# Kernel tuning notes

Hardware: AMD Instinct MI355X
Metric: run time of the kernel (lower is better)

## Reference

```python
import jax, jax.numpy as jnp
import numpy as np

INPUT_DIM = 29
OUTPUT_DIM = 67
ES = 256
HS = 512
SRC_LEN = 64
TRG_LEN = 48
BATCH = 512


def _lstm_cell(x, h, c, Wih, Whh, bih, bhh):
    # PyTorch gate order: i, f, g, o
    g = x @ Wih.T + bih + h @ Whh.T + bhh
    i, f, gg, o = jnp.split(g, 4, axis=-1)
    c_new = jax.nn.sigmoid(f) * c + jax.nn.sigmoid(i) * jnp.tanh(gg)
    h_new = jax.nn.sigmoid(o) * jnp.tanh(c_new)
    return h_new, c_new


def setup_inputs() -> dict:
    key = jax.random.key(0)
    ks = jax.random.split(key, 32)
    s_es = 1.0 / np.sqrt(ES)
    s_hs = 1.0 / np.sqrt(HS)
    inp = {}
    inp['src'] = jax.random.randint(ks[0], (SRC_LEN, BATCH), 0, INPUT_DIM)
    inp['trg'] = jax.random.randint(ks[1], (TRG_LEN, BATCH), 0, OUTPUT_DIM)
    # encoder params
    inp['enc_emb'] = jax.random.normal(ks[2], (INPUT_DIM, ES), jnp.float32)
    inp['enc_Wih_f'] = jax.random.normal(ks[3], (4 * HS, ES), jnp.float32) * s_hs
    inp['enc_Whh_f'] = jax.random.normal(ks[4], (4 * HS, HS), jnp.float32) * s_hs
    inp['enc_bih_f'] = jax.random.normal(ks[5], (4 * HS,), jnp.float32) * s_hs
    inp['enc_bhh_f'] = jax.random.normal(ks[6], (4 * HS,), jnp.float32) * s_hs
    inp['enc_Wih_b'] = jax.random.normal(ks[7], (4 * HS, ES), jnp.float32) * s_hs
    inp['enc_Whh_b'] = jax.random.normal(ks[8], (4 * HS, HS), jnp.float32) * s_hs
    inp['enc_bih_b'] = jax.random.normal(ks[9], (4 * HS,), jnp.float32) * s_hs
    inp['enc_bhh_b'] = jax.random.normal(ks[10], (4 * HS,), jnp.float32) * s_hs
    inp['fc_h_W'] = jax.random.normal(ks[11], (HS, 2 * HS), jnp.float32) * s_hs
    inp['fc_h_b'] = jax.random.normal(ks[12], (HS,), jnp.float32) * s_hs
    inp['fc_c_W'] = jax.random.normal(ks[13], (HS, 2 * HS), jnp.float32) * s_hs
    inp['fc_c_b'] = jax.random.normal(ks[14], (HS,), jnp.float32) * s_hs
    # decoder params
    inp['dec_emb'] = jax.random.normal(ks[15], (OUTPUT_DIM, ES), jnp.float32)
    inp['dec_Wih'] = jax.random.normal(ks[16], (4 * HS, 2 * HS + ES), jnp.float32) * s_hs
    inp['dec_Whh'] = jax.random.normal(ks[17], (4 * HS, HS), jnp.float32) * s_hs
    inp['dec_bih'] = jax.random.normal(ks[18], (4 * HS,), jnp.float32) * s_hs
    inp['dec_bhh'] = jax.random.normal(ks[19], (4 * HS,), jnp.float32) * s_hs
    inp['energy_W'] = jax.random.normal(ks[20], (1, 3 * HS), jnp.float32) * s_hs
    inp['energy_b'] = jax.random.normal(ks[21], (1,), jnp.float32) * s_hs
    inp['fc_out_W'] = jax.random.normal(ks[22], (OUTPUT_DIM, HS), jnp.float32) * s_hs
    inp['fc_out_b'] = jax.random.normal(ks[23], (OUTPUT_DIM,), jnp.float32) * s_hs
    return inp


def _forward(src, trg, enc_emb, enc_Wih_f, enc_Whh_f, enc_bih_f, enc_bhh_f,
             enc_Wih_b, enc_Whh_b, enc_bih_b, enc_bhh_b,
             fc_h_W, fc_h_b, fc_c_W, fc_c_b,
             dec_emb, dec_Wih, dec_Whh, dec_bih, dec_bhh,
             energy_W, energy_b, fc_out_W, fc_out_b):
    S, B = src.shape
    T = trg.shape[0]
    emb = enc_emb[src]  # [S, B, ES]
    h0 = jnp.zeros((B, HS), emb.dtype)
    c0 = jnp.zeros((B, HS), emb.dtype)

    def fwd_step(carry, x_t):
        h, c = carry
        h, c = _lstm_cell(x_t, h, c, enc_Wih_f, enc_Whh_f, enc_bih_f, enc_bhh_f)
        return (h, c), h

    def bwd_step(carry, x_t):
        h, c = carry
        h, c = _lstm_cell(x_t, h, c, enc_Wih_b, enc_Whh_b, enc_bih_b, enc_bhh_b)
        return (h, c), h

    (hf, cf), out_f = jax.lax.scan(fwd_step, (h0, c0), emb)
    (hb, cb), out_b_rev = jax.lax.scan(bwd_step, (h0, c0), emb[::-1])
    out_b = out_b_rev[::-1]
    encoder_states = jnp.concatenate([out_f, out_b], axis=2)  # [S, B, 2H]

    # fc_h / fc_c compress the 2 directions' final hidden/cell to [B, H]
    hidden_h = jnp.concatenate([hf, hb], axis=-1) @ fc_h_W.T + fc_h_b
    hidden_c = jnp.concatenate([cf, cb], axis=-1) @ fc_c_W.T + fc_c_b

    # Attention: original code passes encoder_hidden on EVERY step, so the
    # attention weights and context vector are constant across decode steps.
    h_rep = jnp.broadcast_to(hidden_h[None], (S, B, HS))
    e_in = jnp.concatenate([h_rep, encoder_states], axis=2)  # [S, B, 3H]
    energy = jax.nn.relu(e_in @ energy_W.T + energy_b)  # [S, B, 1]
    attn = jax.nn.softmax(energy, axis=0)[..., 0]  # [S, B]
    context = jnp.einsum('sb,sbh->bh', attn, encoder_states)  # [B, 2H]

    # Decode: teacher_forcing_ratio = 1.0 -> inputs are trg[t-1]; since the
    # rnn initial state is reset to encoder_hidden each step, all T-1 steps
    # are independent and can be computed in parallel.
    dec_in_tok = trg[:-1]  # [T-1, B]
    emb_d = dec_emb[dec_in_tok]  # [T-1, B, ES]
    ctx_rep = jnp.broadcast_to(context[None], (T - 1, B, 2 * HS))
    rnn_in = jnp.concatenate([ctx_rep, emb_d], axis=2)  # [T-1, B, 2H+ES]
    h_new, _ = _lstm_cell(rnn_in, hidden_h[None], hidden_c[None],
                          dec_Wih, dec_Whh, dec_bih, dec_bhh)
    logits = h_new @ fc_out_W.T + fc_out_b  # [T-1, B, V]
    outputs = jnp.concatenate(
        [jnp.zeros((1, B, OUTPUT_DIM), logits.dtype), logits], axis=0)
    return outputs


def reference(src, trg, enc_emb, enc_Wih_f, enc_Whh_f, enc_bih_f, enc_bhh_f,
              enc_Wih_b, enc_Whh_b, enc_bih_b, enc_bhh_b,
              fc_h_W, fc_h_b, fc_c_W, fc_c_b,
              dec_emb, dec_Wih, dec_Whh, dec_bih, dec_bhh,
              energy_W, energy_b, fc_out_W, fc_out_b):
    return _forward(src, trg, enc_emb, enc_Wih_f, enc_Whh_f, enc_bih_f,
                    enc_bhh_f, enc_Wih_b, enc_Whh_b, enc_bih_b, enc_bhh_b,
                    fc_h_W, fc_h_b, fc_c_W, fc_c_b, dec_emb, dec_Wih,
                    dec_Whh, dec_bih, dec_bhh, energy_W, energy_b,
                    fc_out_W, fc_out_b)
```

## Files before the change

### kernel.cpp

```cpp
#include <hip/hip_runtime.h>
#include <cstddef>

#define BATCH 512
#define ESZ   256
#define HSZ   512
#define G4    2048
#define SRCL  64
#define TRGL  48
#define ODIM  67

typedef __bf16  bf8v    __attribute__((ext_vector_type(8)));
typedef float   floatx4 __attribute__((ext_vector_type(4)));

__device__ __forceinline__ floatx4 MF(bf8v a, bf8v b, floatx4 c) {
    return __builtin_amdgcn_mfma_f32_16x16x32_bf16(a, b, c, 0, 0, 0);
}

__device__ __forceinline__ float frcp(float x) { return __builtin_amdgcn_rcpf(x); }
__device__ __forceinline__ float fsig(float x) { return frcp(1.0f + __expf(-x)); }
__device__ __forceinline__ float ftanh(float x) { return 1.0f - 2.0f * frcp(1.0f + __expf(2.0f * x)); }

__device__ __forceinline__ bf8v cvt8(const float* __restrict__ s) {
    float4 a = *(const float4*)s;
    float4 b = *(const float4*)(s + 4);
    bf8v v;
    v[0] = (__bf16)a.x; v[1] = (__bf16)a.y; v[2] = (__bf16)a.z; v[3] = (__bf16)a.w;
    v[4] = (__bf16)b.x; v[5] = (__bf16)b.y; v[6] = (__bf16)b.z; v[7] = (__bf16)b.w;
    return v;
}

__global__ void embed_bf16(const int* __restrict__ tok, const float* __restrict__ table,
                           __bf16* __restrict__ out, int n_rows) {
    int i = blockIdx.x * 256 + threadIdx.x;
    int row = i >> 5;
    if (row >= n_rows) return;
    int e = (i & 31) << 3;
    *(bf8v*)(out + (size_t)row * ESZ + e) = cvt8(table + (size_t)tok[row] * ESZ + e);
}

__global__ void embed_swz(const int* __restrict__ tok, const float* __restrict__ table,
                          __bf16* __restrict__ Az) {
    int i = blockIdx.x * 256 + threadIdx.x;
    int lane = i & 63;
    int kt = (i >> 6) & 7;
    int mt = (i >> 9) & 31;
    int t  = i >> 14;
    int b = mt * 16 + (lane & 15);
    int k = kt * 32 + (lane >> 4) * 8;
    int tk = tok[t * BATCH + b];
    *(bf8v*)(Az + (size_t)i * 8) = cvt8(table + (size_t)tk * ESZ + k);
}

__global__ void zero_kernel(float* __restrict__ p, int n) {
    int i = blockIdx.x * 256 + threadIdx.x;
    if (i < n) p[i] = 0.f;
}

__global__ void bias_prep(const float* __restrict__ af, const float* __restrict__ bf,
                          const float* __restrict__ ab, const float* __restrict__ bb,
                          const float* __restrict__ ad, const float* __restrict__ bd,
                          float* __restrict__ of, float* __restrict__ ob, float* __restrict__ od) {
    int i = blockIdx.x * 256 + threadIdx.x;
    if (i < G4) { of[i] = af[i] + bf[i]; ob[i] = ab[i] + bb[i]; od[i] = ad[i] + bd[i]; }
}

__global__ void wswz_bf16(const float* __restrict__ Wih, const float* __restrict__ Whh,
                          __bf16* __restrict__ Wz) {
    int i = blockIdx.x * 256 + threadIdx.x;
    int lane = i & 63;
    int rest = i >> 6;
    int kt = rest % 24;
    int gj = rest / 24;
    int g = gj & 3, jt = gj >> 2;
    int row = g * 512 + jt * 16 + (lane & 15);
    int k = kt * 32 + (lane >> 4) * 8;
    const float* src = (k < ESZ) ? (Wih + (size_t)row * ESZ + k)
                                 : (Whh + (size_t)row * HSZ + (k - ESZ));
    *(bf8v*)(Wz + (size_t)i * 8) = cvt8(src);
}

__global__ void decw_bf16(const float* __restrict__ dec_Wih, __bf16* __restrict__ We) {
    int i = blockIdx.x * 256 + threadIdx.x;
    int n = i >> 5;
    int e = (i & 31) << 3;
    *(bf8v*)(We + (size_t)n * ESZ + e) =
        cvt8(dec_Wih + (size_t)n * (2 * HSZ + ESZ) + 2 * HSZ + e);
}

__global__ void wdcat_bf16(const float* __restrict__ dec_Wih, const float* __restrict__ dec_Whh,
                           __bf16* __restrict__ Wd) {
    int i = blockIdx.x * 256 + threadIdx.x;
    int n = i / 192;
    int e = (i - n * 192) << 3;
    const float* src = (e < 1024) ? (dec_Wih + (size_t)n * 1280 + e)
                                  : (dec_Whh + (size_t)n * HSZ + (e - 1024));
    *(bf8v*)(Wd + (size_t)n * 1536 + e) = cvt8(src);
}

__global__ void conv_f2b(const float* __restrict__ src, __bf16* __restrict__ dst, int n8) {
    int i = blockIdx.x * 256 + threadIdx.x;
    if (i < n8) *(bf8v*)(dst + (size_t)i * 8) = cvt8(src + (size_t)i * 8);
}

__global__ void fo_pad(const float* __restrict__ W, __bf16* __restrict__ dst) {
    int i = blockIdx.x * 256 + threadIdx.x;
    int r = i >> 6, e = (i & 63) << 3;
    bf8v v;
    if (r < ODIM) v = cvt8(W + (size_t)r * HSZ + e);
    else { for (int k = 0; k < 8; ++k) v[k] = (__bf16)0.f; }
    *(bf8v*)(dst + (size_t)r * HSZ + e) = v;
}

__global__ void cat_hfb(const __bf16* __restrict__ es, __bf16* __restrict__ dst) {
    int i = blockIdx.x * 256 + threadIdx.x;
    int r = i >> 7, e = (i & 127) << 3;
    const __bf16* s = (e < HSZ) ? (es + ((size_t)(63 * BATCH + r)) * 1024 + e)
                                : (es + (size_t)r * 1024 + e);
    *(bf8v*)(dst + (size_t)r * 1024 + e) = *(const bf8v*)s;
}

__global__ void cat_cfb(const float* __restrict__ cbuf, __bf16* __restrict__ dst) {
    int i = blockIdx.x * 256 + threadIdx.x;
    int r = i >> 7, e = (i & 127) << 3;
    const float* s = (e < HSZ) ? (cbuf + (size_t)r * HSZ + e)
                               : (cbuf + (size_t)BATCH * HSZ + (size_t)r * HSZ + (e - HSZ));
    *(bf8v*)(dst + (size_t)r * 1024 + e) = cvt8(s);
}

__global__ void cat_ctxh(const float* __restrict__ ctx, const float* __restrict__ hid_h,
                         __bf16* __restrict__ dst) {
    int i = blockIdx.x * 256 + threadIdx.x;
    int r = i / 192;
    int e = (i - r * 192) << 3;
    const float* s = (e < 1024) ? (ctx + (size_t)r * 1024 + e)
                                : (hid_h + (size_t)r * HSZ + (e - 1024));
    *(bf8v*)(dst + (size_t)r * 1536 + e) = cvt8(s);
}

__global__ void d0_swz(const float* __restrict__ D0, float* __restrict__ D0s) {
    int i = blockIdx.x * 256 + threadIdx.x;
    int b = i >> 11, rest = i & 2047, g = rest >> 9, j = rest & 511;
    D0s[(((size_t)b * 512 + j) << 2) + g] = D0[i];
}

__global__ __launch_bounds__(128) void enc_step5(
    const __bf16* __restrict__ Az, const __bf16* __restrict__ hPrev,
    __bf16* __restrict__ hNext, float* __restrict__ cbuf, __bf16* __restrict__ es,
    const __bf16* __restrict__ WzF, const __bf16* __restrict__ WzB,
    const float* __restrict__ biasF, const float* __restrict__ biasB, int t)
{
    __shared__ float cT[32 * 33];
    __shared__ float hT[32 * 33];

    const int dir = blockIdx.z;
    const int tt  = dir ? (SRCL - 1 - t) : t;
    const __bf16* Wz  = dir ? WzB : WzF;
    const float* bias = dir ? biasB : biasF;
    const int j0 = blockIdx.x * 32;
    const int m0 = blockIdx.y * 32;

    const int tid = threadIdx.x;
    const int w = tid >> 6, lane = tid & 63;
    const int quad = lane >> 4, l15 = lane & 15;
    const int jtw = blockIdx.x * 2 + w;

    {
        int r = tid >> 2, ch = tid & 3;
        const float* cp = cbuf + (size_t)dir * BATCH * HSZ + (size_t)(m0 + r) * HSZ + j0 + ch * 8;
        *(float4*)(&cT[r * 33 + ch * 8])     = *(const float4*)cp;
        *(float4*)(&cT[r * 33 + ch * 8 + 4]) = *(const float4*)(cp + 4);
    }

    floatx4 acc[2][4] = {};
    const int mt0 = m0 >> 4;
    const __bf16* ax0 = Az + ((((size_t)tt * 32 + mt0) * 8) << 9) + lane * 8;
    const __bf16* ax1 = ax0 + (8 << 9);
    const __bf16* ah0 = hPrev + ((((size_t)dir * 32 + mt0) * 16) << 9) + lane * 8;
    const __bf16* ah1 = ah0 + (16 << 9);
    const __bf16* bw  = Wz + (((size_t)jtw * 4 * 24) << 9) + lane * 8;

#pragma unroll 2
    for (int kt = 0; kt < 8; ++kt) {
        bf8v a0 = *(const bf8v*)(ax0 + ((size_t)kt << 9));
        bf8v a1 = *(const bf8v*)(ax1 + ((size_t)kt << 9));
#pragma unroll
        for (int g = 0; g < 4; ++g) {
            bf8v b = *(const bf8v*)(bw + (((size_t)(g * 24 + kt)) << 9));
            acc[0][g] = MF(a0, b, acc[0][g]);
            acc[1][g] = MF(a1, b, acc[1][g]);
        }
    }
#pragma unroll 2
    for (int kt = 0; kt < 16; ++kt) {
        bf8v a0 = *(const bf8v*)(ah0 + ((size_t)kt << 9));
        bf8v a1 = *(const bf8v*)(ah1 + ((size_t)kt << 9));
#pragma unroll
        for (int g = 0; g < 4; ++g) {
            bf8v b = *(const bf8v*)(bw + (((size_t)(g * 24 + 8 + kt)) << 9));
            acc[0][g] = MF(a0, b, acc[0][g]);
            acc[1][g] = MF(a1, b, acc[1][g]);
        }
    }

    __syncthreads();

    const int jl = w * 16 + l15;
    const int j = j0 + jl;
    const float b0 = bias[j], b1 = bias[HSZ + j], b2 = bias[2 * HSZ + j], b3 = bias[3 * HSZ + j];
#pragma unroll
    for (int ms = 0; ms < 2; ++ms) {
#pragma unroll
        for (int r = 0; r < 4; ++r) {
            int ml = ms * 16 + quad * 4 + r;
            float gi = acc[ms][0][r] + b0;
            float gf = acc[ms][1][r] + b1;
            float gg = acc[ms][2][r] + b2;
            float go = acc[ms][3][r] + b3;
            float cn = fsig(gf) * cT[ml * 33 + jl] + fsig(gi) * ftanh(gg);
            cT[ml * 33 + jl] = cn;
            hT[ml * 33 + jl] = fsig(go) * ftanh(cn);
        }
    }
    __syncthreads();

    const size_t cb = (size_t)dir * BATCH * HSZ;
#pragma unroll
    for (int s = 0; s < 2; ++s) {
        int task = tid + s * 128;
        int r = task >> 3, ch = task & 7;
        *(float4*)(cbuf + cb + (size_t)(m0 + r) * HSZ + j0 + ch * 4) =
            *(const float4*)(&cT[r * 33 + ch * 4]);
    }
    {
        int mtl = tid >> 6;
        int ln = tid & 63;
        int q2 = ln >> 4, l2 = ln & 15;
        const float* hp = &hT[(mtl * 16 + l2) * 33 + q2 * 8];
        bf8v v;
#pragma unroll
        for (int e = 0; e < 8; ++e) v[e] = (__bf16)hp[e];
        size_t chunk = ((((size_t)dir * 32 + mt0 + mtl) * 16) + (j0 >> 5)) * 64 + ln;
        *(bf8v*)(hNext + chunk * 8) = v;
    }
    {
        int r = tid >> 2, ch = tid & 3;
        const float* hp = &hT[r * 33 + ch * 8];
        bf8v v;
#pragma unroll
        for (int e = 0; e < 8; ++e) v[e] = (__bf16)hp[e];
        *(bf8v*)(es + ((size_t)tt * BATCH + m0 + r) * 1024 + dir * HSZ + j0 + ch * 8) = v;
    }
}

#define DA_STR 264
__global__ __launch_bounds__(256) void dec_v4(
    const __bf16* __restrict__ embD, const __bf16* __restrict__ We,
    const float* __restrict__ D0s, const float* __restrict__ hidc,
    __bf16* __restrict__ h_new)
{
    __shared__ __bf16 As[128 * DA_STR];
    __shared__ __bf16 Bs2[128 * DA_STR];

    const int m0 = blockIdx.y * 128;
    const int j0 = blockIdx.x * 32;
    const int tid = threadIdx.x;
    const int w = tid >> 6, lane = tid & 63;
    const int quad = lane >> 4, l15 = lane & 15;
    const int mh = (w & 1) * 64;
    const int ghi = w >> 1;
    const int jl = l15 + ghi * 16;

#pragma unroll 4
    for (int i = 0; i < 16; ++i) {
        int idx = tid + i * 256;
        int r = idx >> 5, ch = idx & 31;
        *(bf8v*)(&As[r * DA_STR + ch * 8]) =
            *(const bf8v*)(embD + (size_t)(m0 + r) * ESZ + ch * 8);
        int gate = (r >> 4) & 3;
        int jr = (r & 15) + ((r >> 6) << 4);
        *(bf8v*)(&Bs2[r * DA_STR + ch * 8]) =
            *(const bf8v*)(We + (size_t)(gate * HSZ + j0 + jr) * ESZ + ch * 8);
    }
    __syncthreads();

    floatx4 acc[4][4] = {};
    const __bf16* BhB = &Bs2[(ghi * 64 + l15) * DA_STR + quad * 8];
#pragma unroll 4
    for (int kt = 0; kt < 8; ++kt) {
        bf8v a[4];
#pragma unroll
        for (int ms = 0; ms < 4; ++ms)
            a[ms] = *(const bf8v*)(&As[(mh + ms * 16 + l15) * DA_STR + quad * 8 + kt * 32]);
#pragma unroll
        for (int g = 0; g < 4; ++g) {
            bf8v b = *(const bf8v*)(BhB + g * 16 * DA_STR + kt * 32);
#pragma unroll
            for (int ms = 0; ms < 4; ++ms)
                acc[ms][g] = MF(a[ms], b, acc[ms][g]);
        }
    }

    const int j = j0 + jl;
#pragma unroll
    for (int ms = 0; ms < 4; ++ms) {
        int mr = m0 + mh + ms * 16 + quad * 4;
#pragma unroll
        for (int r = 0; r < 4; ++r) {
            int m = mr + r;
            int b = m & (BATCH - 1);
            floatx4 d0 = *(const floatx4*)(D0s + (((size_t)b * 512 + j) << 2));
            float gi = acc[ms][0][r] + d0[0];
            float gf = acc[ms][1][r] + d0[1];
            float gg = acc[ms][2][r] + d0[2];
            float go = acc[ms][3][r] + d0[3];
            float cn = fsig(gf) * hidc[(size_t)b * HSZ + j] + fsig(gi) * ftanh(gg);
            h_new[(size_t)m * HSZ + j] = (__bf16)(fsig(go) * ftanh(cn));
        }
    }
}

__global__ __launch_bounds__(256) void gmm_bf16(
    const __bf16* __restrict__ A, const __bf16* __restrict__ B, int K,
    const float* __restrict__ bias, float* __restrict__ C, int ldc, int N)
{
    const int tid = threadIdx.x;
    const int w = tid >> 6, lane = tid & 63;
    const int quad = lane >> 4, l15 = lane & 15;
    const int n0 = blockIdx.x * 64;
    const int mA = blockIdx.y * 64 + w * 16 + l15;

    const __bf16* Ar = A + (size_t)mA * K + quad * 8;
    const __bf16* Br[4];
#pragma unroll
    for (int ns = 0; ns < 4; ++ns)
        Br[ns] = B + (size_t)(n0 + ns * 16 + l15) * K + quad * 8;

    floatx4 acc[4] = {};
    const int KT = K >> 5;
#pragma unroll 4
    for (int kt = 0; kt < KT; ++kt) {
        bf8v a = *(const bf8v*)(Ar + kt * 32);
#pragma unroll
        for (int ns = 0; ns < 4; ++ns) {
            bf8v b = *(const bf8v*)(Br[ns] + kt * 32);
            acc[ns] = MF(a, b, acc[ns]);
        }
    }
    const int mb = blockIdx.y * 64 + w * 16 + quad * 4;
#pragma unroll
    for (int ns = 0; ns < 4; ++ns) {
        int n = n0 + ns * 16 + l15;
        if (n < N) {
#pragma unroll
            for (int r = 0; r < 4; ++r)
                C[(size_t)(mb + r) * ldc + n] = acc[ns][r] + bias[n];
        }
    }
}

__global__ void eh_kernel(const float* __restrict__ hid_h, const float* __restrict__ eW,
                          const float* __restrict__ eb, float* __restrict__ eh) {
    int w = blockIdx.x * 4 + (threadIdx.x >> 6);
    int lane = threadIdx.x & 63;
    if (w >= BATCH) return;
    float s = 0.f;
    for (int k = lane; k < HSZ; k += 64) s += hid_h[(size_t)w * HSZ + k] * eW[k];
    for (int off = 32; off; off >>= 1) s += __shfl_down(s, off);
    if (lane == 0) eh[w] = s + eb[0];
}

__global__ void energy_kernel(const __bf16* __restrict__ es, const float* __restrict__ eW2,
                              const float* __restrict__ eh, float* __restrict__ energy) {
    int w = blockIdx.x * 4 + (threadIdx.x >> 6);
    int lane = threadIdx.x & 63;
    int s = w >> 9, b = w & 511;
    const __bf16* row = es + ((size_t)s * BATCH + b) * (2 * HSZ);
    float v = 0.f;
    for (int k = lane; k < 2 * HSZ; k += 64) v += (float)row[k] * eW2[k];
    for (int off = 32; off; off >>= 1) v += __shfl_down(v, off);
    if (lane == 0) energy[(size_t)s * BATCH + b] = fmaxf(v + eh[b], 0.f);
}

__global__ void softmax_kernel(const float* __restrict__ energy, float* __restrict__ attn) {
    int b = blockIdx.x * 4 + (threadIdx.x >> 6);
    int lane = threadIdx.x & 63;
    if (b >= BATCH) return;
    float v = energy[(size_t)lane * BATCH + b];
    float m = v;
    for (int off = 32; off; off >>= 1) m = fmaxf(m, __shfl_xor(m, off));
    float e = __expf(v - m);
    float sum = e;
    for (int off = 32; off; off >>= 1) sum += __shfl_xor(sum, off);
    attn[(size_t)lane * BATCH + b] = e / sum;
}

__global__ void context_kernel(const float* __restrict__ attn, const __bf16* __restrict__ es,
                               float* __restrict__ ctx) {
    int b = blockIdx.x;
    int j = threadIdx.x * 4;
    float a0 = 0.f, a1 = 0.f, a2 = 0.f, a3 = 0.f;
    for (int s = 0; s < SRCL; ++s) {
        float a = attn[(size_t)s * BATCH + b];
        const __bf16* r = es + ((size_t)s * BATCH + b) * (2 * HSZ) + j;
        a0 += a * (float)r[0]; a1 += a * (float)r[1];
        a2 += a * (float)r[2]; a3 += a * (float)r[3];
    }
    float4 o = make_float4(a0, a1, a2, a3);
    *(float4*)(ctx + (size_t)b * (2 * HSZ) + j) = o;
}

extern "C" void kernel_launch(void* const* d_in, const int* in_sizes, int n_in,
                              void* d_out, int out_size, void* d_ws, size_t ws_size,
                              hipStream_t stream) {
    const int*   src      = (const int*)d_in[0];
    const int*   trg      = (const int*)d_in[1];
    const float* enc_emb  = (const float*)d_in[2];
    const float* Wih_f    = (const float*)d_in[3];
    const float* Whh_f    = (const float*)d_in[4];
    const float* bih_f    = (const float*)d_in[5];
    const float* bhh_f    = (const float*)d_in[6];
    const float* Wih_b    = (const float*)d_in[7];
    const float* Whh_b    = (const float*)d_in[8];
    const float* bih_b    = (const float*)d_in[9];
    const float* bhh_b    = (const float*)d_in[10];
    const float* fc_h_W   = (const float*)d_in[11];
    const float* fc_h_b   = (const float*)d_in[12];
    const float* fc_c_W   = (const float*)d_in[13];
    const float* fc_c_b   = (const float*)d_in[14];
    const float* dec_emb  = (const float*)d_in[15];
    const float* dec_Wih  = (const float*)d_in[16];
    const float* dec_Whh  = (const float*)d_in[17];
    const float* dec_bih  = (const float*)d_in[18];
    const float* dec_bhh  = (const float*)d_in[19];
    const float* energy_W = (const float*)d_in[20];
    const float* energy_b = (const float*)d_in[21];
    const float* fc_out_W = (const float*)d_in[22];
    const float* fc_out_b = (const float*)d_in[23];
    float* out = (float*)d_out;

    float* ws = (float*)d_ws;
    size_t o = 0;
    __bf16* Az   = (__bf16*)(ws + o); o += 4194304;
    __bf16* embD = (__bf16*)(ws + o); o += 3080192;
    __bf16* es   = (__bf16*)(ws + o); o += 16777216;
    float* zbase = ws + o;
    __bf16* h0   = (__bf16*)(ws + o); o += 262144;
    __bf16* h1   = (__bf16*)(ws + o); o += 262144;
    float*  cbuf = ws + o;            o += 524288;
    __bf16* WzF  = (__bf16*)(ws + o); o += 786432;
    __bf16* WzB  = (__bf16*)(ws + o); o += 786432;
    __bf16* decWe= (__bf16*)(ws + o); o += 262144;
    __bf16* WdC  = (__bf16*)(ws + o); o += 1572864;
    __bf16* fcWh = (__bf16*)(ws + o); o += 262144;
    __bf16* fcWc = (__bf16*)(ws + o); o += 262144;
    __bf16* foWb = (__bf16*)(ws + o); o += 32768;
    __bf16* hfb  = (__bf16*)(ws + o); o += 262144;
    __bf16* cfb  = (__bf16*)(ws + o); o += 262144;
    __bf16* ctxh = (__bf16*)(ws + o); o += 393216;
    float* hid_h = ws + o;            o += 262144;
    float* hid_c = ws + o;            o += 262144;
    float* ehv   = ws + o;            o += 512;
    float* energy= ws + o;            o += 32768;
    float* attn  = ws + o;            o += 32768;
    float* ctx   = ws + o;            o += 524288;
    float* D0    = ws + o;            o += 1048576;
    float* D0s   = ws + o;            o += 1048576;
    float* bias_f= ws + o;            o += 2048;
    float* bias_b= ws + o;            o += 2048;
    float* bias_d= ws + o;            o += 2048;
    __bf16* h_new= (__bf16*)(ws + o); o += 6160384;

    embed_swz<<<4096, 256, 0, stream>>>(src, enc_emb, Az);
    embed_bf16<<<3008, 256, 0, stream>>>(trg, dec_emb, embD, (TRGL - 1) * BATCH);
    zero_kernel<<<4096, 256, 0, stream>>>(zbase, 1048576);
    bias_prep<<<8, 256, 0, stream>>>(bih_f, bhh_f, bih_b, bhh_b, dec_bih, dec_bhh,
                                     bias_f, bias_b, bias_d);
    wswz_bf16<<<768, 256, 0, stream>>>(Wih_f, Whh_f, WzF);
    wswz_bf16<<<768, 256, 0, stream>>>(Wih_b, Whh_b, WzB);
    decw_bf16<<<256, 256, 0, stream>>>(dec_Wih, decWe);
    wdcat_bf16<<<1536, 256, 0, stream>>>(dec_Wih, dec_Whh, WdC);
    conv_f2b<<<256, 256, 0, stream>>>(fc_h_W, fcWh, 65536);
    conv_f2b<<<256, 256, 0, stream>>>(fc_c_W, fcWc, 65536);
    fo_pad<<<32, 256, 0, stream>>>(fc_out_W, foWb);

    for (int t = 0; t < SRCL; ++t) {
        const __bf16* hp = (t & 1) ? h1 : h0;
        __bf16*       hn = (t & 1) ? h0 : h1;
        enc_step5<<<dim3(16, 16, 2), 128, 0, stream>>>(
            Az, hp, hn, cbuf, es, WzF, WzB, bias_f, bias_b, t);
    }

    cat_hfb<<<256, 256, 0, stream>>>(es, hfb);
    cat_cfb<<<256, 256, 0, stream>>>(cbuf, cfb);
    gmm_bf16<<<dim3(8, 8), 256, 0, stream>>>(hfb, fcWh, 1024, fc_h_b, hid_h, HSZ, HSZ);
    gmm_bf16<<<dim3(8, 8), 256, 0, stream>>>(cfb, fcWc, 1024, fc_c_b, hid_c, HSZ, HSZ);

    eh_kernel<<<128, 256, 0, stream>>>(hid_h, energy_W, energy_b, ehv);
    energy_kernel<<<8192, 256, 0, stream>>>(es, energy_W + HSZ, ehv, energy);
    softmax_kernel<<<128, 256, 0, stream>>>(energy, attn);
    context_kernel<<<512, 256, 0, stream>>>(attn, es, ctx);

    cat_ctxh<<<384, 256, 0, stream>>>(ctx, hid_h, ctxh);
    gmm_bf16<<<dim3(32, 8), 256, 0, stream>>>(ctxh, WdC, 1536, bias_d, D0, G4, G4);
    d0_swz<<<4096, 256, 0, stream>>>(D0, D0s);

    dec_v4<<<dim3(16, 188), 256, 0, stream>>>(embD, decWe, D0s, hid_c, h_new);

    zero_kernel<<<134, 256, 0, stream>>>(out, BATCH * ODIM);
    gmm_bf16<<<dim3(2, 376), 256, 0, stream>>>(h_new, foWb, HSZ, fc_out_b,
                                               out + (size_t)BATCH * ODIM, ODIM, ODIM);
}
```

Baseline: 1.105 ms.

## Pre-swizzle weights into MFMA fragment layout and restage encoder recurrent weights in LDS

Weights and decoder embeddings are rearranged once into MFMA fragment order, so the GEMM and decoder kernels load B and A fragments with coalesced per-lane reads instead of strided row loads or an LDS staging pass. The encoder step kernel now processes 16 hidden units per block with 64 batch rows, stages the recurrent Whh slice in LDS, and updates the cell state directly in global memory. The decoder kernel drops its shared-memory tiles and reads swizzled fragments straight from global memory. This adds several extra one-time swizzle kernels and changes encoder grid shape and occupancy, with more redundant A loads across blocks.

Result: slower. 1.163 ms (+5.3%).

```diff
diff --git a/kernel.cpp b/kernel.cpp
--- a/kernel.cpp
+++ b/kernel.cpp
@@ -10,6 +10,7 @@
 #define ODIM  67
 
 typedef __bf16  bf8v    __attribute__((ext_vector_type(8)));
+typedef __bf16  bf4v    __attribute__((ext_vector_type(4)));
 typedef float   floatx4 __attribute__((ext_vector_type(4)));
 
 __device__ __forceinline__ floatx4 MF(bf8v a, bf8v b, floatx4 c) {
@@ -29,15 +30,6 @@
     return v;
 }
 
-__global__ void embed_bf16(const int* __restrict__ tok, const float* __restrict__ table,
-                           __bf16* __restrict__ out, int n_rows) {
-    int i = blockIdx.x * 256 + threadIdx.x;
-    int row = i >> 5;
-    if (row >= n_rows) return;
-    int e = (i & 31) << 3;
-    *(bf8v*)(out + (size_t)row * ESZ + e) = cvt8(table + (size_t)tok[row] * ESZ + e);
-}
-
 __global__ void embed_swz(const int* __restrict__ tok, const float* __restrict__ table,
                           __bf16* __restrict__ Az) {
     int i = blockIdx.x * 256 + threadIdx.x;
@@ -48,7 +40,20 @@
     int b = mt * 16 + (lane & 15);
     int k = kt * 32 + (lane >> 4) * 8;
     int tk = tok[t * BATCH + b];
+    (void)kt;
     *(bf8v*)(Az + (size_t)i * 8) = cvt8(table + (size_t)tk * ESZ + k);
+}
+
+__global__ void embdz(const int* __restrict__ trg, const float* __restrict__ table,
+                      __bf16* __restrict__ Dz) {
+    int i = blockIdx.x * 256 + threadIdx.x;
+    int lane = i & 63;
+    int kt = (i >> 6) & 7;
+    int mt = i >> 9;
+    int row = mt * 16 + (lane & 15);
+    int k = kt * 32 + (lane >> 4) * 8;
+    int tk = trg[row];
+    *(bf8v*)(Dz + (size_t)i * 8) = cvt8(table + (size_t)tk * ESZ + k);
 }
 
 __global__ void zero_kernel(float* __restrict__ p, int n) {
@@ -79,12 +84,15 @@
     *(bf8v*)(Wz + (size_t)i * 8) = cvt8(src);
 }
 
-__global__ void decw_bf16(const float* __restrict__ dec_Wih, __bf16* __restrict__ We) {
-    int i = blockIdx.x * 256 + threadIdx.x;
-    int n = i >> 5;
-    int e = (i & 31) << 3;
-    *(bf8v*)(We + (size_t)n * ESZ + e) =
-        cvt8(dec_Wih + (size_t)n * (2 * HSZ + ESZ) + 2 * HSZ + e);
+__global__ void decwz(const float* __restrict__ dec_Wih, __bf16* __restrict__ Wz) {
+    int i = blockIdx.x * 256 + threadIdx.x;
+    int lane = i & 63;
+    int kt = (i >> 6) & 7;
+    int nt = i >> 9;
+    int row = nt * 16 + (lane & 15);
+    int k = kt * 32 + (lane >> 4) * 8;
+    *(bf8v*)(Wz + (size_t)i * 8) =
+        cvt8(dec_Wih + (size_t)row * (2 * HSZ + ESZ) + 2 * HSZ + k);
 }
 
 __global__ void wdcat_bf16(const float* __restrict__ dec_Wih, const float* __restrict__ dec_Whh,
@@ -111,6 +119,18 @@
     *(bf8v*)(dst + (size_t)r * HSZ + e) = v;
 }
 
+__global__ void fragswz(const __bf16* __restrict__ src, __bf16* __restrict__ dst,
+                        int KT, int nchunks) {
+    int i = blockIdx.x * 256 + threadIdx.x;
+    if (i >= nchunks) return;
+    int lane = i & 63;
+    int kt = (i >> 6) % KT;
+    int nt = (i >> 6) / KT;
+    int row = nt * 16 + (lane & 15);
+    int k = kt * 32 + (lane >> 4) * 8;
+    *(bf8v*)(dst + (size_t)i * 8) = *(const bf8v*)(src + (size_t)row * (KT * 32) + k);
+}
+
 __global__ void cat_hfb(const __bf16* __restrict__ es, __bf16* __restrict__ dst) {
     int i = blockIdx.x * 256 + threadIdx.x;
     int r = i >> 7, e = (i & 127) << 3;
@@ -143,170 +163,138 @@
     D0s[(((size_t)b * 512 + j) << 2) + g] = D0[i];
 }
 
-__global__ __launch_bounds__(128) void enc_step5(
+__global__ __launch_bounds__(256) void enc_step6(
     const __bf16* __restrict__ Az, const __bf16* __restrict__ hPrev,
     __bf16* __restrict__ hNext, float* __restrict__ cbuf, __bf16* __restrict__ es,
     const __bf16* __restrict__ WzF, const __bf16* __restrict__ WzB,
     const float* __restrict__ biasF, const float* __restrict__ biasB, int t)
 {
-    __shared__ float cT[32 * 33];
-    __shared__ float hT[32 * 33];
+    __shared__ __bf16 Bh[4 * 16 * 64 * 8];
+    __shared__ float  hT[64 * 17];
 
     const int dir = blockIdx.z;
     const int tt  = dir ? (SRCL - 1 - t) : t;
     const __bf16* Wz  = dir ? WzB : WzF;
     const float* bias = dir ? biasB : biasF;
-    const int j0 = blockIdx.x * 32;
-    const int m0 = blockIdx.y * 32;
+    const int jt = blockIdx.x;
+    const int j0 = jt * 16;
+    const int m0 = blockIdx.y * 64;
 
     const int tid = threadIdx.x;
     const int w = tid >> 6, lane = tid & 63;
     const int quad = lane >> 4, l15 = lane & 15;
-    const int jtw = blockIdx.x * 2 + w;
+
+    const __bf16* WzJ = Wz + (((size_t)jt * 4 * 24) << 9);
+
+#pragma unroll
+    for (int it = 0; it < 16; ++it) {
+        int idx = tid + it * 256;
+        *(bf8v*)(Bh + ((size_t)idx << 3)) =
+            *(const bf8v*)(WzJ + (((size_t)(((idx >> 10) * 24 + 8 + ((idx >> 6) & 15)) * 64
+                                            + (idx & 63))) << 3));
+    }
+
+    const int mt = (m0 >> 4) + w;
+    floatx4 acc[4] = {};
+
+    const __bf16* ax = Az + ((((size_t)tt * 32 + mt) * 8) << 9) + lane * 8;
+#pragma unroll
+    for (int kt = 0; kt < 8; ++kt) {
+        bf8v a = *(const bf8v*)(ax + ((size_t)kt << 9));
+#pragma unroll
+        for (int g = 0; g < 4; ++g) {
+            bf8v b = *(const bf8v*)(WzJ + (((size_t)((g * 24 + kt) * 64 + lane)) << 3));
+            acc[g] = MF(a, b, acc[g]);
+        }
+    }
+    __syncthreads();
+    const __bf16* ah = hPrev + ((((size_t)dir * 32 + mt) * 16) << 9) + lane * 8;
+#pragma unroll 4
+    for (int kt = 0; kt < 16; ++kt) {
+        bf8v a = *(const bf8v*)(ah + ((size_t)kt << 9));
+#pragma unroll
+        for (int g = 0; g < 4; ++g) {
+            bf8v b = *(const bf8v*)(Bh + (((size_t)((g * 16 + kt) * 64 + lane)) << 3));
+            acc[g] = MF(a, b, acc[g]);
+        }
+    }
+
+    const int j = j0 + l15;
+    const float b0 = bias[j], b1 = bias[HSZ + j], b2 = bias[2 * HSZ + j], b3 = bias[3 * HSZ + j];
+    const size_t cb = (size_t)dir * BATCH * HSZ;
+    const int mwb = w * 16 + quad * 4;
+#pragma unroll
+    for (int r = 0; r < 4; ++r) {
+        int m = m0 + mwb + r;
+        float gi = acc[0][r] + b0;
+        float gf = acc[1][r] + b1;
+        float gg = acc[2][r] + b2;
+        float go = acc[3][r] + b3;
+        size_t ci = cb + (size_t)m * HSZ + j;
+        float cn = fsig(gf) * cbuf[ci] + fsig(gi) * ftanh(gg);
+        cbuf[ci] = cn;
+        hT[(mwb + r) * 17 + l15] = fsig(go) * ftanh(cn);
+    }
+    __syncthreads();
 
     {
         int r = tid >> 2, ch = tid & 3;
-        const float* cp = cbuf + (size_t)dir * BATCH * HSZ + (size_t)(m0 + r) * HSZ + j0 + ch * 8;
-        *(float4*)(&cT[r * 33 + ch * 8])     = *(const float4*)cp;
-        *(float4*)(&cT[r * 33 + ch * 8 + 4]) = *(const float4*)(cp + 4);
-    }
-
-    floatx4 acc[2][4] = {};
-    const int mt0 = m0 >> 4;
-    const __bf16* ax0 = Az + ((((size_t)tt * 32 + mt0) * 8) << 9) + lane * 8;
-    const __bf16* ax1 = ax0 + (8 << 9);
-    const __bf16* ah0 = hPrev + ((((size_t)dir * 32 + mt0) * 16) << 9) + lane * 8;
-    const __bf16* ah1 = ah0 + (16 << 9);
-    const __bf16* bw  = Wz + (((size_t)jtw * 4 * 24) << 9) + lane * 8;
-
-#pragma unroll 2
-    for (int kt = 0; kt < 8; ++kt) {
-        bf8v a0 = *(const bf8v*)(ax0 + ((size_t)kt << 9));
-        bf8v a1 = *(const bf8v*)(ax1 + ((size_t)kt << 9));
-#pragma unroll
-        for (int g = 0; g < 4; ++g) {
-            bf8v b = *(const bf8v*)(bw + (((size_t)(g * 24 + kt)) << 9));
-            acc[0][g] = MF(a0, b, acc[0][g]);
-            acc[1][g] = MF(a1, b, acc[1][g]);
-        }
-    }
-#pragma unroll 2
-    for (int kt = 0; kt < 16; ++kt) {
-        bf8v a0 = *(const bf8v*)(ah0 + ((size_t)kt << 9));
-        bf8v a1 = *(const bf8v*)(ah1 + ((size_t)kt << 9));
-#pragma unroll
-        for (int g = 0; g < 4; ++g) {
-            bf8v b = *(const bf8v*)(bw + (((size_t)(g * 24 + 8 + kt)) << 9));
-            acc[0][g] = MF(a0, b, acc[0][g]);
-            acc[1][g] = MF(a1, b, acc[1][g]);
-        }
-    }
-
-    __syncthreads();
-
-    const int jl = w * 16 + l15;
-    const int j = j0 + jl;
-    const float b0 = bias[j], b1 = bias[HSZ + j], b2 = bias[2 * HSZ + j], b3 = bias[3 * HSZ + j];
-#pragma unroll
-    for (int ms = 0; ms < 2; ++ms) {
-#pragma unroll
-        for (int r = 0; r < 4; ++r) {
-            int ml = ms * 16 + quad * 4 + r;
-            float gi = acc[ms][0][r] + b0;
-            float gf = acc[ms][1][r] + b1;
-            float gg = acc[ms][2][r] + b2;
-            float go = acc[ms][3][r] + b3;
-            float cn = fsig(gf) * cT[ml * 33 + jl] + fsig(gi) * ftanh(gg);
-            cT[ml * 33 + jl] = cn;
-            hT[ml * 33 + jl] = fsig(go) * ftanh(cn);
-        }
-    }
-    __syncthreads();
-
-    const size_t cb = (size_t)dir * BATCH * HSZ;
-#pragma unroll
-    for (int s = 0; s < 2; ++s) {
-        int task = tid + s * 128;
-        int r = task >> 3, ch = task & 7;
-        *(float4*)(cbuf + cb + (size_t)(m0 + r) * HSZ + j0 + ch * 4) =
-            *(const float4*)(&cT[r * 33 + ch * 4]);
-    }
-    {
-        int mtl = tid >> 6;
-        int ln = tid & 63;
-        int q2 = ln >> 4, l2 = ln & 15;
-        const float* hp = &hT[(mtl * 16 + l2) * 33 + q2 * 8];
+        const float* hp = &hT[r * 17 + ch * 4];
+        bf4v v;
+#pragma unroll
+        for (int e = 0; e < 4; ++e) v[e] = (__bf16)hp[e];
+        *(bf4v*)(es + ((size_t)tt * BATCH + m0 + r) * 1024 + dir * HSZ + j0 + ch * 4) = v;
+    }
+    if (tid < 128) {
+        int mtl = tid >> 5;
+        int lnsub = tid & 31;
+        int jhalf = (j0 >> 4) & 1;
+        int ln = lnsub + jhalf * 32;
+        int mloc = mtl * 16 + (lnsub & 15);
+        int jloc = (lnsub >> 4) * 8;
+        const float* hp = &hT[mloc * 17 + jloc];
         bf8v v;
 #pragma unroll
         for (int e = 0; e < 8; ++e) v[e] = (__bf16)hp[e];
-        size_t chunk = ((((size_t)dir * 32 + mt0 + mtl) * 16) + (j0 >> 5)) * 64 + ln;
+        size_t chunk = (((size_t)dir * 32 + (m0 >> 4) + mtl) * 16 + (j0 >> 5)) * 64 + ln;
         *(bf8v*)(hNext + chunk * 8) = v;
     }
-    {
-        int r = tid >> 2, ch = tid & 3;
-        const float* hp = &hT[r * 33 + ch * 8];
-        bf8v v;
-#pragma unroll
-        for (int e = 0; e < 8; ++e) v[e] = (__bf16)hp[e];
-        *(bf8v*)(es + ((size_t)tt * BATCH + m0 + r) * 1024 + dir * HSZ + j0 + ch * 8) = v;
-    }
-}
-
-#define DA_STR 264
-__global__ __launch_bounds__(256) void dec_v4(
-    const __bf16* __restrict__ embD, const __bf16* __restrict__ We,
+}
+
+__global__ __launch_bounds__(256) void dec_v6(
+    const __bf16* __restrict__ Dz, const __bf16* __restrict__ Wz,
     const float* __restrict__ D0s, const float* __restrict__ hidc,
     __bf16* __restrict__ h_new)
 {
-    __shared__ __bf16 As[128 * DA_STR];
-    __shared__ __bf16 Bs2[128 * DA_STR];
-
-    const int m0 = blockIdx.y * 128;
-    const int j0 = blockIdx.x * 32;
     const int tid = threadIdx.x;
     const int w = tid >> 6, lane = tid & 63;
     const int quad = lane >> 4, l15 = lane & 15;
-    const int mh = (w & 1) * 64;
-    const int ghi = w >> 1;
-    const int jl = l15 + ghi * 16;
-
-#pragma unroll 4
-    for (int i = 0; i < 16; ++i) {
-        int idx = tid + i * 256;
-        int r = idx >> 5, ch = idx & 31;
-        *(bf8v*)(&As[r * DA_STR + ch * 8]) =
-            *(const bf8v*)(embD + (size_t)(m0 + r) * ESZ + ch * 8);
-        int gate = (r >> 4) & 3;
-        int jr = (r & 15) + ((r >> 6) << 4);
-        *(bf8v*)(&Bs2[r * DA_STR + ch * 8]) =
-            *(const bf8v*)(We + (size_t)(gate * HSZ + j0 + jr) * ESZ + ch * 8);
-    }
-    __syncthreads();
+    const int jt = blockIdx.x;
+    const int mt0 = blockIdx.y * 16 + w * 4;
 
     floatx4 acc[4][4] = {};
-    const __bf16* BhB = &Bs2[(ghi * 64 + l15) * DA_STR + quad * 8];
-#pragma unroll 4
+    const __bf16* az = Dz + (((size_t)mt0 * 8) << 9) + lane * 8;
+#pragma unroll
     for (int kt = 0; kt < 8; ++kt) {
         bf8v a[4];
 #pragma unroll
         for (int ms = 0; ms < 4; ++ms)
-            a[ms] = *(const bf8v*)(&As[(mh + ms * 16 + l15) * DA_STR + quad * 8 + kt * 32]);
+            a[ms] = *(const bf8v*)(az + (((size_t)(ms * 8 + kt)) << 9));
 #pragma unroll
         for (int g = 0; g < 4; ++g) {
-            bf8v b = *(const bf8v*)(BhB + g * 16 * DA_STR + kt * 32);
+            bf8v b = *(const bf8v*)(Wz + (((size_t)(((g * 32 + jt) * 8 + kt) * 64 + lane)) << 3));
 #pragma unroll
             for (int ms = 0; ms < 4; ++ms)
                 acc[ms][g] = MF(a[ms], b, acc[ms][g]);
         }
     }
-
-    const int j = j0 + jl;
+    const int j = jt * 16 + l15;
 #pragma unroll
     for (int ms = 0; ms < 4; ++ms) {
-        int mr = m0 + mh + ms * 16 + quad * 4;
+        int mb = (mt0 + ms) * 16 + quad * 4;
 #pragma unroll
         for (int r = 0; r < 4; ++r) {
-            int m = mr + r;
+            int m = mb + r;
             int b = m & (BATCH - 1);
             floatx4 d0 = *(const floatx4*)(D0s + (((size_t)b * 512 + j) << 2));
             float gi = acc[ms][0][r] + d0[0];
@@ -319,8 +307,8 @@
     }
 }
 
-__global__ __launch_bounds__(256) void gmm_bf16(
-    const __bf16* __restrict__ A, const __bf16* __restrict__ B, int K,
+__global__ __launch_bounds__(256) void gmmz(
+    const __bf16* __restrict__ A, const __bf16* __restrict__ Bz, int K, int KT,
     const float* __restrict__ bias, float* __restrict__ C, int ldc, int N)
 {
     const int tid = threadIdx.x;
@@ -328,21 +316,15 @@
     const int quad = lane >> 4, l15 = lane & 15;
     const int n0 = blockIdx.x * 64;
     const int mA = blockIdx.y * 64 + w * 16 + l15;
-
     const __bf16* Ar = A + (size_t)mA * K + quad * 8;
-    const __bf16* Br[4];
-#pragma unroll
-    for (int ns = 0; ns < 4; ++ns)
-        Br[ns] = B + (size_t)(n0 + ns * 16 + l15) * K + quad * 8;
 
     floatx4 acc[4] = {};
-    const int KT = K >> 5;
-#pragma unroll 4
     for (int kt = 0; kt < KT; ++kt) {
         bf8v a = *(const bf8v*)(Ar + kt * 32);
 #pragma unroll
         for (int ns = 0; ns < 4; ++ns) {
-            bf8v b = *(const bf8v*)(Br[ns] + kt * 32);
+            int jt = (n0 >> 4) + ns;
+            bf8v b = *(const bf8v*)(Bz + (((size_t)((jt * KT + kt) * 64 + lane)) << 3));
             acc[ns] = MF(a, b, acc[ns]);
         }
     }
@@ -441,7 +423,7 @@
     float* ws = (float*)d_ws;
     size_t o = 0;
     __bf16* Az   = (__bf16*)(ws + o); o += 4194304;
-    __bf16* embD = (__bf16*)(ws + o); o += 3080192;
+    __bf16* Dz   = (__bf16*)(ws + o); o += 3080192;
     __bf16* es   = (__bf16*)(ws + o); o += 16777216;
     float* zbase = ws + o;
     __bf16* h0   = (__bf16*)(ws + o); o += 262144;
@@ -449,11 +431,15 @@
     float*  cbuf = ws + o;            o += 524288;
     __bf16* WzF  = (__bf16*)(ws + o); o += 786432;
     __bf16* WzB  = (__bf16*)(ws + o); o += 786432;
-    __bf16* decWe= (__bf16*)(ws + o); o += 262144;
+    __bf16* decWzp=(__bf16*)(ws + o); o += 262144;
     __bf16* WdC  = (__bf16*)(ws + o); o += 1572864;
+    __bf16* WdZ  = (__bf16*)(ws + o); o += 1572864;
     __bf16* fcWh = (__bf16*)(ws + o); o += 262144;
+    __bf16* fcWhZ= (__bf16*)(ws + o); o += 262144;
     __bf16* fcWc = (__bf16*)(ws + o); o += 262144;
+    __bf16* fcWcZ= (__bf16*)(ws + o); o += 262144;
     __bf16* foWb = (__bf16*)(ws + o); o += 32768;
+    __bf16* foWz = (__bf16*)(ws + o); o += 32768;
     __bf16* hfb  = (__bf16*)(ws + o); o += 262144;
     __bf16* cfb  = (__bf16*)(ws + o); o += 262144;
     __bf16* ctxh = (__bf16*)(ws + o); o += 393216;
@@ -471,29 +457,33 @@
     __bf16* h_new= (__bf16*)(ws + o); o += 6160384;
 
     embed_swz<<<4096, 256, 0, stream>>>(src, enc_emb, Az);
-    embed_bf16<<<3008, 256, 0, stream>>>(trg, dec_emb, embD, (TRGL - 1) * BATCH);
+    embdz<<<3008, 256, 0, stream>>>(trg, dec_emb, Dz);
     zero_kernel<<<4096, 256, 0, stream>>>(zbase, 1048576);
     bias_prep<<<8, 256, 0, stream>>>(bih_f, bhh_f, bih_b, bhh_b, dec_bih, dec_bhh,
                                      bias_f, bias_b, bias_d);
     wswz_bf16<<<768, 256, 0, stream>>>(Wih_f, Whh_f, WzF);
     wswz_bf16<<<768, 256, 0, stream>>>(Wih_b, Whh_b, WzB);
-    decw_bf16<<<256, 256, 0, stream>>>(dec_Wih, decWe);
+    decwz<<<256, 256, 0, stream>>>(dec_Wih, decWzp);
     wdcat_bf16<<<1536, 256, 0, stream>>>(dec_Wih, dec_Whh, WdC);
+    fragswz<<<1536, 256, 0, stream>>>(WdC, WdZ, 48, 393216);
     conv_f2b<<<256, 256, 0, stream>>>(fc_h_W, fcWh, 65536);
+    fragswz<<<256, 256, 0, stream>>>(fcWh, fcWhZ, 32, 65536);
     conv_f2b<<<256, 256, 0, stream>>>(fc_c_W, fcWc, 65536);
+    fragswz<<<256, 256, 0, stream>>>(fcWc, fcWcZ, 32, 65536);
     fo_pad<<<32, 256, 0, stream>>>(fc_out_W, foWb);
+    fragswz<<<32, 256, 0, stream>>>(foWb, foWz, 16, 8192);
 
     for (int t = 0; t < SRCL; ++t) {
         const __bf16* hp = (t & 1) ? h1 : h0;
         __bf16*       hn = (t & 1) ? h0 : h1;
-        enc_step5<<<dim3(16, 16, 2), 128, 0, stream>>>(
+        enc_step6<<<dim3(32, 8, 2), 256, 0, stream>>>(
             Az, hp, hn, cbuf, es, WzF, WzB, bias_f, bias_b, t);
     }
 
     cat_hfb<<<256, 256, 0, stream>>>(es, hfb);
     cat_cfb<<<256, 256, 0, stream>>>(cbuf, cfb);
-    gmm_bf16<<<dim3(8, 8), 256, 0, stream>>>(hfb, fcWh, 1024, fc_h_b, hid_h, HSZ, HSZ);
-    gmm_bf16<<<dim3(8, 8), 256, 0, stream>>>(cfb, fcWc, 1024, fc_c_b, hid_c, HSZ, HSZ);
+    gmmz<<<dim3(8, 8), 256, 0, stream>>>(hfb, fcWhZ, 1024, 32, fc_h_b, hid_h, HSZ, HSZ);
+    gmmz<<<dim3(8, 8), 256, 0, stream>>>(cfb, fcWcZ, 1024, 32, fc_c_b, hid_c, HSZ, HSZ);
 
     eh_kernel<<<128, 256, 0, stream>>>(hid_h, energy_W, energy_b, ehv);
     energy_kernel<<<8192, 256, 0, stream>>>(es, energy_W + HSZ, ehv, energy);
@@ -501,12 +491,12 @@
     context_kernel<<<512, 256, 0, stream>>>(attn, es, ctx);
 
     cat_ctxh<<<384, 256, 0, stream>>>(ctx, hid_h, ctxh);
-    gmm_bf16<<<dim3(32, 8), 256, 0, stream>>>(ctxh, WdC, 1536, bias_d, D0, G4, G4);
+    gmmz<<<dim3(32, 8), 256, 0, stream>>>(ctxh, WdZ, 1536, 48, bias_d, D0, G4, G4);
     d0_swz<<<4096, 256, 0, stream>>>(D0, D0s);
 
-    dec_v4<<<dim3(16, 188), 256, 0, stream>>>(embD, decWe, D0s, hid_c, h_new);
+    dec_v6<<<dim3(32, 94), 256, 0, stream>>>(Dz, decWzp, D0s, hid_c, h_new);
 
     zero_kernel<<<134, 256, 0, stream>>>(out, BATCH * ODIM);
-    gmm_bf16<<<dim3(2, 376), 256, 0, stream>>>(h_new, foWb, HSZ, fc_out_b,
-                                               out + (size_t)BATCH * ODIM, ODIM, ODIM);
-}
+    gmmz<<<dim3(2, 376), 256, 0, stream>>>(h_new, foWz, HSZ, 16, fc_out_b,
+                                           out + (size_t)BATCH * ODIM, ODIM, ODIM);
+}
```
